# Kernel tuning notes

Measured on AMD Instinct MI355X. Metric: run time of the kernel, lower is better.

Reference implementation:

```python
import jax, jax.numpy as jnp
import numpy as np
import math

NUM_HEADS = 16
ROPE_BASE = 10000.0
SLIDING_WINDOW = 512  # note: original triu-then-tril composition makes the mask empty (no-op)


def _rope_cos_sin(seq_len, head_dim, dtype):
    inv_freq = 1.0 / (ROPE_BASE ** (jnp.arange(0, head_dim, 2, dtype=jnp.float32) / head_dim))
    t = jnp.arange(seq_len, dtype=jnp.float32)
    freqs = t[:, None] * inv_freq[None, :]          # [S, D/2]
    emb = jnp.concatenate([freqs, freqs], axis=-1)  # [S, D]
    # reshape to broadcast over [B, S, H, D]
    return jnp.cos(emb)[None, :, None, :].astype(dtype), jnp.sin(emb)[None, :, None, :].astype(dtype)


def _rotate_half(x):
    x1, x2 = jnp.split(x, 2, axis=-1)
    return jnp.concatenate([-x2, x1], axis=-1)


def setup_inputs() -> dict:
    key = jax.random.key(0)
    ks = jax.random.split(key, 9)
    B, S, E = 2, 2048, 2048
    sc = 1.0 / math.sqrt(E)
    return {
        "hidden_states": jax.random.normal(ks[0], (B, S, E), dtype=jnp.float32),
        "Wq": jax.random.normal(ks[1], (E, E), dtype=jnp.float32) * sc,
        "bq": jax.random.normal(ks[2], (E,), dtype=jnp.float32) * 0.01,
        "Wk": jax.random.normal(ks[3], (E, E), dtype=jnp.float32) * sc,
        "bk": jax.random.normal(ks[4], (E,), dtype=jnp.float32) * 0.01,
        "Wv": jax.random.normal(ks[5], (E, E), dtype=jnp.float32) * sc,
        "bv": jax.random.normal(ks[6], (E,), dtype=jnp.float32) * 0.01,
        "Wo": jax.random.normal(ks[7], (E, E), dtype=jnp.float32) * sc,
        "bo": jax.random.normal(ks[8], (E,), dtype=jnp.float32) * 0.01,
    }


def reference(hidden_states, Wq, bq, Wk, bk, Wv, bv, Wo, bo):
    B, S, E = hidden_states.shape
    H = NUM_HEADS
    D = E // H
    q = (hidden_states @ Wq.T + bq).reshape(B, S, H, D)
    k = (hidden_states @ Wk.T + bk).reshape(B, S, H, D)
    v = (hidden_states @ Wv.T + bv).reshape(B, S, H, D)

    cos, sin = _rope_cos_sin(S, D, q.dtype)
    q = q * cos + _rotate_half(q) * sin
    k = k * cos + _rotate_half(k) * sin

    scale = 1.0 / math.sqrt(D)
    scores = jnp.einsum("bqhd,bkhd->bhqk", q, k) * scale  # [B,H,S,S]
    # Faithful to source: triu(ones, +w) followed by tril(..., -w) is empty -> mask is a no-op.
    attn = jax.nn.softmax(scores, axis=-1)
    out = jnp.einsum("bhqk,bkhd->bqhd", attn, v).reshape(B, S, E)
    return out @ Wo.T + bo
```

## Files before the change

kernel.cpp:

```cpp
#include <hip/hip_runtime.h>
#include <hip/hip_bf16.h>

#define B_ 2
#define S_ 2048
#define E_ 2048
#define H_ 16
#define D_ 128
#define M_ (B_*S_)
#define NQKV_ (3*E_)

typedef __attribute__((ext_vector_type(8))) short bf16x8;
typedef __attribute__((ext_vector_type(4))) float f32x4;
typedef __attribute__((ext_vector_type(4))) unsigned short u16x4;
typedef __attribute__((ext_vector_type(2))) unsigned u32x2;

__device__ __forceinline__ unsigned short f2bf(float f) {
  union { float f; unsigned u; } v; v.f = f;
  unsigned r = v.u + 0x7fffu + ((v.u >> 16) & 1u);
  return (unsigned short)(r >> 16);
}
__device__ __forceinline__ float bf2f(unsigned short h) {
  union { unsigned u; float f; } v; v.u = ((unsigned)h) << 16;
  return v.f;
}

__device__ __forceinline__ void gload_lds16(const void* g, void* l) {
  __builtin_amdgcn_global_load_lds(
      (const __attribute__((address_space(1))) unsigned*)g,
      (__attribute__((address_space(3))) unsigned*)l, 16, 0, 0);
}

__global__ __launch_bounds__(256) void prep_kernel(
    const float* __restrict__ hs,
    const float* __restrict__ Wq, const float* __restrict__ Wk, const float* __restrict__ Wv,
    const float* __restrict__ Wo,
    const float* __restrict__ bq, const float* __restrict__ bk, const float* __restrict__ bv,
    unsigned short* __restrict__ hsb, unsigned short* __restrict__ Wqkv,
    unsigned short* __restrict__ Wob, float* __restrict__ biasqkv,
    float* __restrict__ cosT, float* __restrict__ sinT)
{
  const int seg = blockIdx.y;
  const int t0 = blockIdx.x * 256 + threadIdx.x;
  const int stride = gridDim.x * 256;
  if (seg == 0) {
    const int n = (M_*E_)/4;
    for (int i = t0; i < n; i += stride) {
      f32x4 v = ((const f32x4*)hs)[i];
      u16x4 o; o[0]=f2bf(v[0]); o[1]=f2bf(v[1]); o[2]=f2bf(v[2]); o[3]=f2bf(v[3]);
      ((u16x4*)hsb)[i] = o;
    }
  } else if (seg == 1) {
    const int n = (3*E_*E_)/4;
    for (int i = t0; i < n; i += stride) {
      int e4 = i << 2;
      int r = e4 >> 11;
      int k = e4 & 2047;
      const float* src = (r < E_) ? (Wq + ((size_t)r << 11) + k)
                       : (r < 2*E_) ? (Wk + ((size_t)(r - E_) << 11) + k)
                       : (Wv + ((size_t)(r - 2*E_) << 11) + k);
      f32x4 v = *(const f32x4*)src;
      u16x4 o; o[0]=f2bf(v[0]); o[1]=f2bf(v[1]); o[2]=f2bf(v[2]); o[3]=f2bf(v[3]);
      ((u16x4*)Wqkv)[i] = o;
    }
  } else if (seg == 2) {
    const int n = (E_*E_)/4;
    for (int i = t0; i < n; i += stride) {
      f32x4 v = ((const f32x4*)Wo)[i];
      u16x4 o; o[0]=f2bf(v[0]); o[1]=f2bf(v[1]); o[2]=f2bf(v[2]); o[3]=f2bf(v[3]);
      ((u16x4*)Wob)[i] = o;
    }
  } else if (seg == 3) {
    for (int i = t0; i < NQKV_; i += stride)
      biasqkv[i] = (i < E_) ? bq[i] : (i < 2*E_) ? bk[i - E_] : bv[i - 2*E_];
  } else {
    for (int i = t0; i < S_*64; i += stride) {
      int j = i & 63, s = i >> 6;
      float inv = exp2f(-(float)j * (13.287712379549449f / 64.0f));
      float ang = (float)s * inv;
      cosT[i] = cosf(ang);
      sinT[i] = sinf(ang);
    }
  }
}

template<int OUT_F32>
__global__ __launch_bounds__(256) void gemm_bt(
    const unsigned short* __restrict__ A,
    const unsigned short* __restrict__ Bm,
    const float* __restrict__ bias,
    void* __restrict__ Cv,
    int M, int N, int K)
{
  __shared__ unsigned short lA[128*64];
  __shared__ unsigned short lB[128*64];
  const int tid = threadIdx.x;
  const int lane = tid & 63;
  const int w = tid >> 6;
  const int wr = w >> 1, wc = w & 1;
  const int ntile = N >> 7;
  const int tm = blockIdx.x / ntile, tn = blockIdx.x % ntile;
  const int l15 = lane & 15, l4 = lane >> 4;

  f32x4 acc[4][4] = {};

  for (int kt = 0; kt < K; kt += 64) {
    #pragma unroll
    for (int i = 0; i < 4; ++i) {
      int cc = i*256 + tid;
      int row = cc >> 3, col = cc & 7;
      int scol = col ^ (row & 7);
      gload_lds16(A + (size_t)(tm*128 + row)*K + kt + scol*8, (char*)lA + cc*16);
    }
    #pragma unroll
    for (int i = 0; i < 4; ++i) {
      int cc = i*256 + tid;
      int row = cc >> 3, col = cc & 7;
      int scol = col ^ (row & 7);
      gload_lds16(Bm + (size_t)(tn*128 + row)*K + kt + scol*8, (char*)lB + cc*16);
    }
    asm volatile("s_waitcnt vmcnt(0)" ::: "memory");
    __syncthreads();

    #pragma unroll
    for (int ks = 0; ks < 2; ++ks) {
      bf16x8 af[4], bfr[4];
      #pragma unroll
      for (int mt = 0; mt < 4; ++mt) {
        int row = wr*64 + mt*16 + l15;
        int ch = (ks*4 + l4) ^ (row & 7);
        af[mt] = *(const bf16x8*)(lA + row*64 + ch*8);
      }
      #pragma unroll
      for (int nt = 0; nt < 4; ++nt) {
        int row = wc*64 + nt*16 + l15;
        int ch = (ks*4 + l4) ^ (row & 7);
        bfr[nt] = *(const bf16x8*)(lB + row*64 + ch*8);
      }
      #pragma unroll
      for (int mt = 0; mt < 4; ++mt)
        #pragma unroll
        for (int nt = 0; nt < 4; ++nt)
          acc[mt][nt] = __builtin_amdgcn_mfma_f32_16x16x32_bf16(af[mt], bfr[nt], acc[mt][nt], 0, 0, 0);
    }
    __syncthreads();
  }

  #pragma unroll
  for (int mt = 0; mt < 4; ++mt) {
    #pragma unroll
    for (int nt = 0; nt < 4; ++nt) {
      int colg = tn*128 + wc*64 + nt*16 + l15;
      float bvv = bias[colg];
      #pragma unroll
      for (int r = 0; r < 4; ++r) {
        int rowg = tm*128 + wr*64 + mt*16 + l4*4 + r;
        float v = acc[mt][nt][r] + bvv;
        if (OUT_F32) ((float*)Cv)[(size_t)rowg*N + colg] = v;
        else ((unsigned short*)Cv)[(size_t)rowg*N + colg] = f2bf(v);
      }
    }
  }
}

__global__ __launch_bounds__(256) void rope_kernel(
    unsigned short* __restrict__ qkv, const float* __restrict__ cosT, const float* __restrict__ sinT)
{
  int t = blockIdx.x*256 + threadIdx.x;
  int i  = t & 63;
  int h  = (t >> 6) & 15;
  int m  = t >> 10;
  int s  = m & (S_-1);
  float c = cosT[s*64 + i], sn = sinT[s*64 + i];
  const float scale = 0.08838834764831845f * 1.4426950408889634f;
  size_t base = (size_t)m*NQKV_ + h*128;
  float q1 = bf2f(qkv[base+i]), q2 = bf2f(qkv[base+64+i]);
  qkv[base+i]    = f2bf((q1*c - q2*sn)*scale);
  qkv[base+64+i] = f2bf((q2*c + q1*sn)*scale);
  size_t kb = base + E_;
  float k1 = bf2f(qkv[kb+i]), k2 = bf2f(qkv[kb+64+i]);
  qkv[kb+i]    = f2bf(k1*c - k2*sn);
  qkv[kb+64+i] = f2bf(k2*c + k1*sn);
}

__global__ __launch_bounds__(256) void transv_kernel(
    const unsigned short* __restrict__ qkv, unsigned short* __restrict__ Vt)
{
  __shared__ unsigned short t[32][33];
  int bid = blockIdx.x;
  int st = bid & 63;
  int dt = (bid >> 6) & 3;
  int bh = bid >> 8;
  int b = bh >> 4, h = bh & 15;
  int tx = threadIdx.x & 31, ty = threadIdx.x >> 5;
  #pragma unroll
  for (int j = 0; j < 4; ++j) {
    int r = ty + j*8;
    t[r][tx] = qkv[(size_t)(b*S_ + st*32 + r)*NQKV_ + 2*E_ + h*128 + dt*32 + tx];
  }
  __syncthreads();
  #pragma unroll
  for (int j = 0; j < 4; ++j) {
    int r = ty + j*8;
    Vt[((size_t)bh*D_ + dt*32 + r)*S_ + st*32 + tx] = t[tx][r];
  }
}

__global__ __launch_bounds__(256, 4) void attn_kernel(
    const unsigned short* __restrict__ qkv, const unsigned short* __restrict__ Vt,
    unsigned short* __restrict__ Ao)
{
  __shared__ unsigned short lK[64*128];
  __shared__ unsigned short lV[128*64];
  __shared__ __align__(16) unsigned short lP[4*16*64];
  const int bid = blockIdx.x;
  const int qt = bid & 31;
  const int bh = bid >> 5;
  const int b = bh >> 4, h = bh & 15;
  const int tid = threadIdx.x, lane = tid & 63, w = tid >> 6;
  const int l15 = lane & 15, l4 = lane >> 4;

  const int qrow = qt*64 + w*16 + l15;
  const unsigned short* qp = qkv + (size_t)(b*S_ + qrow)*NQKV_ + h*128 + l4*8;
  bf16x8 qf[4];
  #pragma unroll
  for (int f = 0; f < 4; ++f) qf[f] = *(const bf16x8*)(qp + f*32);

  f32x4 O[8];
  #pragma unroll
  for (int i = 0; i < 8; ++i) O[i] = (f32x4){0.f,0.f,0.f,0.f};
  float m = -1e30f, lsum = 0.f;

  unsigned short* myP = lP + w*(16*64);
  const int ksw = (l15 & 7) << 3;
  const size_t kbase = (size_t)b*S_*NQKV_ + E_ + (size_t)h*128;
  const size_t vbase = (size_t)bh*D_*S_;

  for (int kt = 0; kt < S_; kt += 64) {
    #pragma unroll
    for (int i = 0; i < 4; ++i) {
      int cc = i*256 + tid;
      int row = cc >> 4, col = cc & 15;
      int scol = col ^ (row & 7);
      gload_lds16(qkv + kbase + (size_t)(kt + row)*NQKV_ + scol*8, (char*)lK + cc*16);
    }
    #pragma unroll
    for (int i = 0; i < 4; ++i) {
      int cc = i*256 + tid;
      int row = cc >> 3, col = cc & 7;
      int scol = col ^ ((row & 7) ^ ((row >> 3) & 7));
      gload_lds16(Vt + vbase + (size_t)row*S_ + kt + scol*8, (char*)lV + cc*16);
    }
    asm volatile("s_waitcnt vmcnt(0)" ::: "memory");
    __syncthreads();

    f32x4 sfr[4];
    #pragma unroll
    for (int nf = 0; nf < 4; ++nf) {
      f32x4 s = (f32x4){0.f,0.f,0.f,0.f};
      #pragma unroll
      for (int ks = 0; ks < 4; ++ks) {
        int row = nf*16 + l15;
        int ch = (ks*4 + l4) ^ (row & 7);
        bf16x8 kf = *(const bf16x8*)(lK + row*128 + ch*8);
        s = __builtin_amdgcn_mfma_f32_16x16x32_bf16(kf, qf[ks], s, 0, 0, 0);
      }
      sfr[nf] = s;
    }

    float vmax = -1e30f;
    #pragma unroll
    for (int nf = 0; nf < 4; ++nf)
      #pragma unroll
      for (int r = 0; r < 4; ++r) vmax = fmaxf(vmax, sfr[nf][r]);
    vmax = fmaxf(vmax, __shfl_xor(vmax, 16, 64));
    vmax = fmaxf(vmax, __shfl_xor(vmax, 32, 64));

    if (__any(vmax > m + 8.0f)) {
      float mn = fmaxf(m, vmax);
      float al = __builtin_amdgcn_exp2f(m - mn);
      m = mn;
      lsum *= al;
      #pragma unroll
      for (int r = 0; r < 4; ++r) {
        float ar = __shfl(al, (lane & 48) + l4*4 + r, 64);
        #pragma unroll
        for (int df = 0; df < 8; ++df) O[df][r] *= ar;
      }
    }

    float ps = 0.f;
    #pragma unroll
    for (int nf = 0; nf < 4; ++nf) {
      #pragma unroll
      for (int r = 0; r < 4; ++r) {
        float p = __builtin_amdgcn_exp2f(sfr[nf][r] - m);
        sfr[nf][r] = p;
        ps += p;
      }
    }
    ps += __shfl_xor(ps, 16, 64);
    ps += __shfl_xor(ps, 32, 64);
    lsum += ps;

    #pragma unroll
    for (int nf = 0; nf < 4; ++nf) {
      unsigned lo = (unsigned)f2bf(sfr[nf][0]) | ((unsigned)f2bf(sfr[nf][1]) << 16);
      unsigned hi = (unsigned)f2bf(sfr[nf][2]) | ((unsigned)f2bf(sfr[nf][3]) << 16);
      int k0 = (nf*16 + l4*4) ^ ksw;
      u32x2 val; val[0] = lo; val[1] = hi;
      *(u32x2*)(myP + l15*64 + k0) = val;
    }
    asm volatile("s_waitcnt lgkmcnt(0)" ::: "memory");

    #pragma unroll
    for (int ks2 = 0; ks2 < 2; ++ks2) {
      int kk = (ks2*32 + l4*8) ^ ksw;
      bf16x8 pf = *(const bf16x8*)(myP + l15*64 + kk);
      #pragma unroll
      for (int df = 0; df < 8; ++df) {
        int row = df*16 + l15;
        int ch = (ks2*4 + l4) ^ ((row & 7) ^ ((row >> 3) & 7));
        bf16x8 vf = *(const bf16x8*)(lV + row*64 + ch*8);
        O[df] = __builtin_amdgcn_mfma_f32_16x16x32_bf16(pf, vf, O[df], 0, 0, 0);
      }
    }
    __syncthreads();
  }

  float linv = 1.0f / lsum;
  float inv[4];
  #pragma unroll
  for (int r = 0; r < 4; ++r) inv[r] = __shfl(linv, (lane & 48) + l4*4 + r, 64);
  #pragma unroll
  for (int df = 0; df < 8; ++df) {
    int colg = h*128 + df*16 + l15;
    #pragma unroll
    for (int r = 0; r < 4; ++r) {
      int rowg = qt*64 + w*16 + l4*4 + r;
      Ao[(size_t)(b*S_ + rowg)*E_ + colg] = f2bf(O[df][r] * inv[r]);
    }
  }
}

extern "C" void kernel_launch(void* const* d_in, const int* in_sizes, int n_in,
                              void* d_out, int out_size, void* d_ws, size_t ws_size,
                              hipStream_t stream) {
  const float* hs = (const float*)d_in[0];
  const float* Wq = (const float*)d_in[1];
  const float* bq = (const float*)d_in[2];
  const float* Wk = (const float*)d_in[3];
  const float* bk = (const float*)d_in[4];
  const float* Wv = (const float*)d_in[5];
  const float* bv = (const float*)d_in[6];
  const float* Wo = (const float*)d_in[7];
  const float* bo = (const float*)d_in[8];
  float* out = (float*)d_out;

  char* p = (char*)d_ws;
  auto alloc = [&](size_t bytes) { char* r = p; p += (bytes + 255) & ~(size_t)255; return r; };
  unsigned short* hsb  = (unsigned short*)alloc((size_t)M_*E_*2);
  unsigned short* Wqkv = (unsigned short*)alloc((size_t)NQKV_*E_*2);
  unsigned short* Wob  = (unsigned short*)alloc((size_t)E_*E_*2);
  unsigned short* qkv  = (unsigned short*)alloc((size_t)M_*NQKV_*2);
  unsigned short* Vt   = (unsigned short*)alloc((size_t)B_*H_*D_*S_*2);
  unsigned short* Ao   = (unsigned short*)alloc((size_t)M_*E_*2);
  float* biasqkv = (float*)alloc((size_t)NQKV_*4);
  float* cosT = (float*)alloc((size_t)S_*64*4);
  float* sinT = (float*)alloc((size_t)S_*64*4);

  prep_kernel<<<dim3(2048, 5), 256, 0, stream>>>(hs, Wq, Wk, Wv, Wo, bq, bk, bv,
      hsb, Wqkv, Wob, biasqkv, cosT, sinT);
  gemm_bt<0><<<dim3((M_/128)*(NQKV_/128)), 256, 0, stream>>>(hsb, Wqkv, biasqkv, qkv, M_, NQKV_, E_);
  rope_kernel<<<dim3((M_*H_*64)/256), 256, 0, stream>>>(qkv, cosT, sinT);
  transv_kernel<<<dim3(B_*H_*(D_/32)*(S_/32)), 256, 0, stream>>>(qkv, Vt);
  attn_kernel<<<dim3(B_*H_*(S_/64)), 256, 0, stream>>>(qkv, Vt, Ao);
  gemm_bt<1><<<dim3((M_/128)*(E_/128)), 256, 0, stream>>>(Ao, Wob, bo, out, M_, E_, E_);
}
```

Measured before the change: 323.4 us.

## Replace GEMM with triple-buffered async-LDS pipeline and 256x128 tiles

Both projection GEMMs now use a kernel that keeps three LDS stages in flight with a K-step of 32. Loads for step j+2 are issued while step j computes, with vmcnt-based waits replacing the full drain-and-sync per iteration. The tile grows to 256x128, giving each wave 8x4 MFMA accumulators for more reuse. The XOR swizzle is dropped, so LDS reads may hit bank conflicts, and the larger accumulator raises register pressure under the launch_bounds(256,2) hint. The grid also halves, leaving fewer blocks to fill the CUs.

```diff
diff --git a/kernel.cpp b/kernel.cpp
--- a/kernel.cpp
+++ b/kernel.cpp
@@ -84,15 +84,15 @@
 }
 
 template<int OUT_F32>
-__global__ __launch_bounds__(256) void gemm_bt(
+__global__ __launch_bounds__(256, 2) void gemm_pipe(
     const unsigned short* __restrict__ A,
     const unsigned short* __restrict__ Bm,
     const float* __restrict__ bias,
     void* __restrict__ Cv,
     int M, int N, int K)
 {
-  __shared__ unsigned short lA[128*64];
-  __shared__ unsigned short lB[128*64];
+  __shared__ __align__(16) unsigned short lA[3][256*32];
+  __shared__ __align__(16) unsigned short lB[3][128*32];
   const int tid = threadIdx.x;
   const int lane = tid & 63;
   const int w = tid >> 6;
@@ -100,60 +100,69 @@
   const int ntile = N >> 7;
   const int tm = blockIdx.x / ntile, tn = blockIdx.x % ntile;
   const int l15 = lane & 15, l4 = lane >> 4;
-
-  f32x4 acc[4][4] = {};
-
-  for (int kt = 0; kt < K; kt += 64) {
+  const int NT = K >> 5;
+
+  const unsigned short* Abase = A + ((size_t)tm*256)*K;
+  const unsigned short* Bbase = Bm + ((size_t)tn*128)*K;
+
+  f32x4 acc[8][4] = {};
+
+  auto stage = [&](int bs, int kt) {
+    const unsigned short* Ag = Abase + kt*32;
     #pragma unroll
     for (int i = 0; i < 4; ++i) {
-      int cc = i*256 + tid;
-      int row = cc >> 3, col = cc & 7;
-      int scol = col ^ (row & 7);
-      gload_lds16(A + (size_t)(tm*128 + row)*K + kt + scol*8, (char*)lA + cc*16);
-    }
-    #pragma unroll
-    for (int i = 0; i < 4; ++i) {
-      int cc = i*256 + tid;
-      int row = cc >> 3, col = cc & 7;
-      int scol = col ^ (row & 7);
-      gload_lds16(Bm + (size_t)(tn*128 + row)*K + kt + scol*8, (char*)lB + cc*16);
-    }
-    asm volatile("s_waitcnt vmcnt(0)" ::: "memory");
-    __syncthreads();
-
-    #pragma unroll
-    for (int ks = 0; ks < 2; ++ks) {
-      bf16x8 af[4], bfr[4];
-      #pragma unroll
-      for (int mt = 0; mt < 4; ++mt) {
-        int row = wr*64 + mt*16 + l15;
-        int ch = (ks*4 + l4) ^ (row & 7);
-        af[mt] = *(const bf16x8*)(lA + row*64 + ch*8);
-      }
-      #pragma unroll
-      for (int nt = 0; nt < 4; ++nt) {
-        int row = wc*64 + nt*16 + l15;
-        int ch = (ks*4 + l4) ^ (row & 7);
-        bfr[nt] = *(const bf16x8*)(lB + row*64 + ch*8);
-      }
-      #pragma unroll
-      for (int mt = 0; mt < 4; ++mt)
-        #pragma unroll
-        for (int nt = 0; nt < 4; ++nt)
-          acc[mt][nt] = __builtin_amdgcn_mfma_f32_16x16x32_bf16(af[mt], bfr[nt], acc[mt][nt], 0, 0, 0);
-    }
-    __syncthreads();
-  }
-
-  #pragma unroll
-  for (int mt = 0; mt < 4; ++mt) {
+      int cc = i*256 + tid; int row = cc >> 2, col = cc & 3;
+      gload_lds16(Ag + (size_t)row*K + col*8, (char*)(&lA[bs][0]) + cc*16);
+    }
+    const unsigned short* Bg = Bbase + kt*32;
+    #pragma unroll
+    for (int i = 0; i < 2; ++i) {
+      int cc = i*256 + tid; int row = cc >> 2, col = cc & 3;
+      gload_lds16(Bg + (size_t)row*K + col*8, (char*)(&lB[bs][0]) + cc*16);
+    }
+  };
+
+  stage(0, 0);
+  stage(1, 1);
+
+  int bufj = 0;
+  for (int j = 0; j < NT; ++j) {
+    __builtin_amdgcn_sched_barrier(0);
+    asm volatile("s_waitcnt lgkmcnt(0)" ::: "memory");
+    if (j == NT-1) asm volatile("s_waitcnt vmcnt(0)" ::: "memory");
+    else           asm volatile("s_waitcnt vmcnt(6)" ::: "memory");
+    __builtin_amdgcn_s_barrier();
+    __builtin_amdgcn_sched_barrier(0);
+    if (j + 2 < NT) {
+      int bs = bufj + 2; if (bs >= 3) bs -= 3;
+      stage(bs, j + 2);
+    }
+    const unsigned short* la = &lA[bufj][0];
+    const unsigned short* lb = &lB[bufj][0];
+    bf16x8 af[8], bfr[4];
+    #pragma unroll
+    for (int mt = 0; mt < 8; ++mt)
+      af[mt] = *(const bf16x8*)(la + (wr*128 + mt*16 + l15)*32 + l4*8);
+    #pragma unroll
+    for (int nt = 0; nt < 4; ++nt)
+      bfr[nt] = *(const bf16x8*)(lb + (wc*64 + nt*16 + l15)*32 + l4*8);
+    #pragma unroll
+    for (int mt = 0; mt < 8; ++mt)
+      #pragma unroll
+      for (int nt = 0; nt < 4; ++nt)
+        acc[mt][nt] = __builtin_amdgcn_mfma_f32_16x16x32_bf16(af[mt], bfr[nt], acc[mt][nt], 0, 0, 0);
+    ++bufj; if (bufj == 3) bufj = 0;
+  }
+
+  #pragma unroll
+  for (int mt = 0; mt < 8; ++mt) {
     #pragma unroll
     for (int nt = 0; nt < 4; ++nt) {
       int colg = tn*128 + wc*64 + nt*16 + l15;
       float bvv = bias[colg];
       #pragma unroll
       for (int r = 0; r < 4; ++r) {
-        int rowg = tm*128 + wr*64 + mt*16 + l4*4 + r;
+        int rowg = tm*256 + wr*128 + mt*16 + l4*4 + r;
         float v = acc[mt][nt][r] + bvv;
         if (OUT_F32) ((float*)Cv)[(size_t)rowg*N + colg] = v;
         else ((unsigned short*)Cv)[(size_t)rowg*N + colg] = f2bf(v);
@@ -370,9 +379,9 @@
 
   prep_kernel<<<dim3(2048, 5), 256, 0, stream>>>(hs, Wq, Wk, Wv, Wo, bq, bk, bv,
       hsb, Wqkv, Wob, biasqkv, cosT, sinT);
-  gemm_bt<0><<<dim3((M_/128)*(NQKV_/128)), 256, 0, stream>>>(hsb, Wqkv, biasqkv, qkv, M_, NQKV_, E_);
+  gemm_pipe<0><<<dim3((M_/256)*(NQKV_/128)), 256, 0, stream>>>(hsb, Wqkv, biasqkv, qkv, M_, NQKV_, E_);
   rope_kernel<<<dim3((M_*H_*64)/256), 256, 0, stream>>>(qkv, cosT, sinT);
   transv_kernel<<<dim3(B_*H_*(D_/32)*(S_/32)), 256, 0, stream>>>(qkv, Vt);
   attn_kernel<<<dim3(B_*H_*(S_/64)), 256, 0, stream>>>(qkv, Vt, Ao);
-  gemm_bt<1><<<dim3((M_/128)*(E_/128)), 256, 0, stream>>>(Ao, Wob, bo, out, M_, E_, E_);
-}
+  gemm_pipe<1><<<dim3((M_/256)*(E_/128)), 256, 0, stream>>>(Ao, Wob, bo, out, M_, E_, E_);
+}
```

Result: slower. 363.9 us (+12.5%).

## Replace QKV GEMM with 256x256-tile 8-wave pipelined kernel

Applied to the files above, without the earlier changes.

Adds a new bf16 GEMM kernel that uses 256x256 output tiles with 512 threads, double-buffered LDS filled by direct global-to-LDS loads, and XOR-swizzled layout. The K loop is split into eight phases that interleave async staging of the next tiles with MFMA work, using explicit waitcnts, barriers and priority bumps. It also remaps workgroups across XCDs. The goal is more data reuse per tile and better overlap of memory loads with matrix math for the largest GEMM. The cost is higher register and LDS pressure and tight dependence on hand-tuned wait counts.

```diff
diff --git a/kernel.cpp b/kernel.cpp
--- a/kernel.cpp
+++ b/kernel.cpp
@@ -79,6 +79,125 @@
       float ang = (float)s * inv;
       cosT[i] = cosf(ang);
       sinT[i] = sinf(ang);
+    }
+  }
+}
+
+#define STAGE8(basePtr, BUF, AB, KS, KT) do { \
+    unsigned short* dst_ = lds + (BUF)*32768 + (AB)*16384 + (KS)*8192; \
+    const unsigned short* src_ = (basePtr) + (KT)*64 + (KS)*32; \
+    _Pragma("unroll") \
+    for (int j_ = 0; j_ < 2; ++j_) { \
+      int cc_ = (j_ << 9) + tid; \
+      int row_ = cc_ >> 2, c2_ = cc_ & 3; \
+      int sc_ = c2_ ^ ((row_ >> 1) & 3); \
+      gload_lds16(src_ + (size_t)row_*K + sc_*8, (char*)dst_ + cc_*16); \
+    } } while(0)
+
+#define LOADA8(MH, KS, BUF) do { \
+    const unsigned short* Ab_ = lds + (BUF)*32768 + (KS)*8192; \
+    _Pragma("unroll") \
+    for (int j_ = 0; j_ < 4; ++j_) { \
+      int row_ = wr*128 + ((MH)*4 + j_)*16 + l15; \
+      af[j_] = *(const bf16x8*)(Ab_ + row_*32 + ((l4 ^ ((row_>>1)&3)) << 3)); \
+    } } while(0)
+
+#define LOADB8(KS, BUF) do { \
+    const unsigned short* Bb_ = lds + (BUF)*32768 + 16384 + (KS)*8192; \
+    _Pragma("unroll") \
+    for (int j_ = 0; j_ < 4; ++j_) { \
+      int row_ = wc*64 + j_*16 + l15; \
+      bf[j_] = *(const bf16x8*)(Bb_ + row_*32 + ((l4 ^ ((row_>>1)&3)) << 3)); \
+    } } while(0)
+
+#define MFMAQ8(MH) do { \
+    _Pragma("unroll") \
+    for (int mm_ = 0; mm_ < 4; ++mm_) \
+      _Pragma("unroll") \
+      for (int nn_ = 0; nn_ < 4; ++nn_) \
+        acc[(MH)*4+mm_][nn_] = __builtin_amdgcn_mfma_f32_16x16x32_bf16(af[mm_], bf[nn_], acc[(MH)*4+mm_][nn_], 0,0,0); \
+    } while(0)
+
+#define VMW6 do { if (nl) asm volatile("s_waitcnt vmcnt(6)" ::: "memory"); \
+                  else    asm volatile("s_waitcnt vmcnt(0)" ::: "memory"); } while(0)
+#define VMNONE do {} while(0)
+
+#define PHASE8(MH, KS, BUF, ISSUE, WAITV) do { \
+    LOADA8(MH, KS, BUF); \
+    if ((MH) == 0) LOADB8(KS, BUF); \
+    ISSUE; \
+    __builtin_amdgcn_sched_barrier(0); \
+    __builtin_amdgcn_s_barrier(); \
+    asm volatile("s_waitcnt lgkmcnt(0)" ::: "memory"); \
+    __builtin_amdgcn_sched_barrier(0); \
+    __builtin_amdgcn_s_setprio(1); \
+    MFMAQ8(MH); \
+    __builtin_amdgcn_s_setprio(0); \
+    __builtin_amdgcn_sched_barrier(0); \
+    WAITV; \
+    __builtin_amdgcn_s_barrier(); \
+  } while(0)
+
+__global__ __launch_bounds__(512, 2) void gemm8(
+    const unsigned short* __restrict__ A,
+    const unsigned short* __restrict__ Bm,
+    const float* __restrict__ bias,
+    unsigned short* __restrict__ Cv,
+    int M, int N, int K)
+{
+  __shared__ __align__(16) unsigned short lds[65536];
+  const int tid = threadIdx.x;
+  const int lane = tid & 63;
+  const int w = tid >> 6;
+  const int wr = w >> 2, wc = w & 3;
+  const int l15 = lane & 15, l4 = lane >> 4;
+
+  const int ntile = N >> 8;
+  int wg = blockIdx.x;
+  const int cpx = gridDim.x >> 3;
+  wg = (wg & 7) * cpx + (wg >> 3);
+  const int tm = wg / ntile, tn = wg % ntile;
+
+  const unsigned short* Abase = A + ((size_t)tm*256)*K;
+  const unsigned short* Bbase = Bm + ((size_t)tn*256)*K;
+
+  f32x4 acc[8][4] = {};
+  bf16x8 af[4], bf[4];
+
+  const int NITER = K >> 7;
+
+  STAGE8(Bbase, 0, 1, 0, 0); STAGE8(Abase, 0, 0, 0, 0);
+  STAGE8(Bbase, 0, 1, 1, 0); STAGE8(Abase, 0, 0, 1, 0);
+  STAGE8(Bbase, 1, 1, 0, 1); STAGE8(Abase, 1, 0, 0, 1);
+  STAGE8(Bbase, 1, 1, 1, 1);
+  __builtin_amdgcn_sched_barrier(0);
+  asm volatile("s_waitcnt vmcnt(6)" ::: "memory");
+  __builtin_amdgcn_s_barrier();
+
+  for (int i = 0; i < NITER; ++i) {
+    const int t1k = 2*i + 1, t2k = 2*i + 2, t3k = 2*i + 3;
+    const bool nl = (i < NITER - 1);
+    PHASE8(0, 0, 0, STAGE8(Abase, 1, 0, 1, t1k), VMNONE);
+    PHASE8(1, 0, 0, if (nl) STAGE8(Bbase, 0, 1, 0, t2k), VMNONE);
+    PHASE8(0, 1, 0, if (nl) STAGE8(Abase, 0, 0, 0, t2k), VMNONE);
+    PHASE8(1, 1, 0, if (nl) STAGE8(Bbase, 0, 1, 1, t2k), VMW6);
+    PHASE8(0, 0, 1, if (nl) STAGE8(Abase, 0, 0, 1, t2k), VMNONE);
+    PHASE8(1, 0, 1, if (nl) STAGE8(Bbase, 1, 1, 0, t3k), VMNONE);
+    PHASE8(0, 1, 1, if (nl) STAGE8(Abase, 1, 0, 0, t3k), VMNONE);
+    PHASE8(1, 1, 1, if (nl) STAGE8(Bbase, 1, 1, 1, t3k), VMW6);
+  }
+
+  #pragma unroll
+  for (int mt = 0; mt < 8; ++mt) {
+    #pragma unroll
+    for (int nt = 0; nt < 4; ++nt) {
+      int colg = tn*256 + wc*64 + nt*16 + l15;
+      float bvv = bias[colg];
+      #pragma unroll
+      for (int r = 0; r < 4; ++r) {
+        int rowg = tm*256 + wr*128 + mt*16 + l4*4 + r;
+        Cv[(size_t)rowg*N + colg] = f2bf(acc[mt][nt][r] + bvv);
+      }
     }
   }
 }
@@ -370,7 +489,7 @@
 
   prep_kernel<<<dim3(2048, 5), 256, 0, stream>>>(hs, Wq, Wk, Wv, Wo, bq, bk, bv,
       hsb, Wqkv, Wob, biasqkv, cosT, sinT);
-  gemm_bt<0><<<dim3((M_/128)*(NQKV_/128)), 256, 0, stream>>>(hsb, Wqkv, biasqkv, qkv, M_, NQKV_, E_);
+  gemm8<<<dim3((M_/256)*(NQKV_/256)), 512, 0, stream>>>(hsb, Wqkv, biasqkv, qkv, M_, NQKV_, E_);
   rope_kernel<<<dim3((M_*H_*64)/256), 256, 0, stream>>>(qkv, cosT, sinT);
   transv_kernel<<<dim3(B_*H_*(D_/32)*(S_/32)), 256, 0, stream>>>(qkv, Vt);
   attn_kernel<<<dim3(B_*H_*(S_/64)), 256, 0, stream>>>(qkv, Vt, Ao);
```

After: 319.0 us. Within noise of the previous version (-1.4%).
